# Optimization experiments

Measured on AMD Instinct MI355X. Metric: run time of the kernel, lower is better.

The kernel has to match this reference:

```python
import jax, jax.numpy as jnp
import numpy as np

DN = ('NCHW', 'OIHW', 'NCHW')
TEMP = 3.0
EPS = 1e-5


def conv2d(x, w, b):
    y = jax.lax.conv_general_dilated(x, w, (1, 1), 'SAME', dimension_numbers=DN)
    return y + b[None, :, None, None]


def cp_conv4d(x, wq, bq, wsp, bsp):
    # CenterPivotConv4d: 2D conv over query dims (h,w) batched over support dims,
    # plus 2D conv over support dims (hs,ws) batched over query dims.
    B, C, h, w, hs, ws = x.shape
    x1 = x.transpose(0, 4, 5, 1, 2, 3).reshape(B * hs * ws, C, h, w)
    o1 = conv2d(x1, wq, bq)
    Co = o1.shape[1]
    o1 = o1.reshape(B, hs, ws, Co, h, w).transpose(0, 3, 4, 5, 1, 2)
    x2 = x.transpose(0, 2, 3, 1, 4, 5).reshape(B * h * w, C, hs, ws)
    o2 = conv2d(x2, wsp, bsp)
    o2 = o2.reshape(B, h, w, Co, hs, ws).transpose(0, 3, 1, 2, 4, 5)
    return o1 + o2


def conv_stack(x, params):
    for wq, bq, wsp, bsp in params:  # fixed 3 layers, structurally distinct channels
        x = jax.nn.relu(cp_conv4d(x, wq, bq, wsp, bsp))
    return x


def neigh_consensus(x, params):
    # symmetric_mode: conv(x) + conv(x with (h,w)<->(hs,ws) swapped), swapped back
    y1 = conv_stack(x, params)
    y2 = conv_stack(x.transpose(0, 1, 4, 5, 2, 3), params).transpose(0, 1, 4, 5, 2, 3)
    return y1 + y2


def mutual_matching(c):
    # c: [B, 1, f1, f2, f3, f4]; ch==1 so the torch views reduce to axis maxes
    b_max = jnp.max(c, axis=(1, 2, 3), keepdims=True)  # max over (ch,f1,f2) per (f3,f4)
    a_max = jnp.max(c, axis=(4, 5), keepdims=True)     # max over (f3,f4) per (f1,f2)
    return c * (c / (a_max + EPS)) * (c / (b_max + EPS))


def matchnet_fwd(corr, v, ig_mask, params):
    B, _, h, w, hs, ws = corr.shape
    c = mutual_matching(corr)
    c = neigh_consensus(c, params)
    c = mutual_matching(c)
    corr2d = c.reshape(B, h * w, hs * ws)
    mask = jnp.broadcast_to(ig_mask.reshape(B, -1, hs * ws), corr2d.shape)
    corr2d = jnp.where(mask, jnp.float32(1e-4), corr2d)
    attn = jax.nn.softmax(corr2d * TEMP, axis=-1)
    # bmm(v, attn^T): v [B,Cv,K], attn [B,Q,K] -> [B,Cv,Q]
    wv = jnp.einsum('bck,bqk->bcq', v, attn)
    return wv.reshape(B, -1, h, w)


def setup_inputs():
    key = jax.random.key(0)
    ks = jax.random.split(key, 16)
    B, h, w, hs, ws, Cv = 4, 32, 32, 32, 32, 256
    chans = [(1, 10), (10, 10), (10, 1)]
    inp = {
        'corr': jax.random.normal(ks[0], (B, 1, h, w, hs, ws), jnp.float32),
        'v': jax.random.normal(ks[1], (B, Cv, hs * ws), jnp.float32),
        'ig_mask': jax.random.bernoulli(ks[2], 0.1, (B, 1, hs * ws)),
    }
    i = 3
    for li, (ci, co) in enumerate(chans):
        inp[f'wq{li}'] = jax.random.normal(ks[i], (co, ci, 3, 3), jnp.float32) * 0.1; i += 1
        inp[f'bq{li}'] = jax.random.normal(ks[i], (co,), jnp.float32) * 0.01; i += 1
        inp[f'ws{li}'] = jax.random.normal(ks[i], (co, ci, 3, 3), jnp.float32) * 0.1; i += 1
        inp[f'bs{li}'] = jax.random.normal(ks[i], (co,), jnp.float32) * 0.01; i += 1
    return inp


def reference(corr, v, ig_mask, wq0, bq0, ws0, bs0, wq1, bq1, ws1, bs1, wq2, bq2, ws2, bs2):
    params = [(wq0, bq0, ws0, bs0), (wq1, bq1, ws1, bs1), (wq2, bq2, ws2, bs2)]
    return matchnet_fwd(corr, v, ig_mask, params)
```

## Files before the change

### kernel.cpp

```cpp
#include <hip/hip_runtime.h>
#include <hip/hip_bf16.h>
#include <cstdint>

#define TEMPF 3.0f
#define EPSF 1e-5f

typedef __attribute__((ext_vector_type(8))) short bf16x8;
typedef __attribute__((ext_vector_type(4))) float f32x4;

static __device__ __forceinline__ float bf2f(unsigned short u){
  union { unsigned u32; float f; } x; x.u32 = ((unsigned)u) << 16; return x.f;
}
static __device__ __forceinline__ unsigned short f2bf(float f){
  unsigned u = __float_as_uint(f);
  unsigned r = (u + 0x7fffu + ((u >> 16) & 1u)) >> 16;
  return (unsigned short)r;
}
static __device__ __forceinline__ float4 ld4(const float* p){ return *(const float4*)p; }
static __device__ __forceinline__ float4 ld4(const __hip_bfloat16* p){
  ushort4 u = *(const ushort4*)p;
  return make_float4(bf2f(u.x), bf2f(u.y), bf2f(u.z), bf2f(u.w));
}
static __device__ __forceinline__ void st4(float* p, float4 v){ *(float4*)p = v; }
static __device__ __forceinline__ void st4(__hip_bfloat16* p, float4 v){
  *(ushort4*)p = make_ushort4(f2bf(v.x), f2bf(v.y), f2bf(v.z), f2bf(v.w));
}

static __device__ __forceinline__ unsigned fkey(float f){
  unsigned u = __float_as_uint(f);
  return (u & 0x80000000u) ? ~u : (u | 0x80000000u);
}
static __device__ __forceinline__ float fdec(unsigned k){
  return (k & 0x80000000u) ? __uint_as_float(k ^ 0x80000000u) : __uint_as_float(~k);
}

__device__ __forceinline__ float blockMax256(float v){
  __shared__ float red[4];
  #pragma unroll
  for(int off = 32; off; off >>= 1) v = fmaxf(v, __shfl_down(v, off));
  __syncthreads();
  if((threadIdx.x & 63) == 0) red[threadIdx.x >> 6] = v;
  __syncthreads();
  return fmaxf(fmaxf(red[0], red[1]), fmaxf(red[2], red[3]));
}
__device__ __forceinline__ float blockSum256(float v){
  __shared__ float red2[4];
  #pragma unroll
  for(int off = 32; off; off >>= 1) v += __shfl_down(v, off);
  __syncthreads();
  if((threadIdx.x & 63) == 0) red2[threadIdx.x >> 6] = v;
  __syncthreads();
  return red2[0] + red2[1] + red2[2] + red2[3];
}

__global__ void detect_k(const unsigned* __restrict__ m, int* __restrict__ flag){
  __shared__ int sa, sb;
  int tid = threadIdx.x;
  if(tid == 0){ sa = 0; sb = 0; }
  __syncthreads();
  int a = 0, b2 = 0;
  for(int i = tid; i < 1024; i += 256){
    unsigned w = m[i];
    if(w != 0u && w != 1u) a = 1;
    if(w != 0u && w != 0x3f800000u) b2 = 1;
  }
  if(a)  atomicOr(&sa, 1);
  if(b2) atomicOr(&sb, 1);
  __syncthreads();
  if(tid == 0) *flag = (sa == 0) ? 0 : ((sb == 0) ? 1 : 2);
}

__global__ void zero_k(unsigned* a, unsigned* b, unsigned* z){
  int i = blockIdx.x * 256 + threadIdx.x;
  if(i < 4096){ a[i] = 0u; b[i] = 0u; }
  if(i < 1024) z[i] = 0u;
}

__global__ __launch_bounds__(256) void zeroy_k(float4* __restrict__ y){
  y[blockIdx.x * 256 + threadIdx.x] = make_float4(0.f, 0.f, 0.f, 0.f);
}

__global__ __launch_bounds__(256) void rowmax_k(const float* __restrict__ x,
                                                float* __restrict__ rmax){
  int row = blockIdx.x;
  float4 v = *(const float4*)(x + (size_t)row * 1024 + threadIdx.x * 4);
  float m = fmaxf(fmaxf(v.x, v.y), fmaxf(v.z, v.w));
  m = blockMax256(m);
  if(threadIdx.x == 0) rmax[row] = m;
}

__global__ __launch_bounds__(256) void colmax_k(const float* __restrict__ x,
                                                unsigned* __restrict__ cbits){
  int blk = blockIdx.x;
  int b = blk >> 5, rg = blk & 31;
  const float* base = x + (size_t)b * 1024 * 1024 + (size_t)rg * 32 * 1024;
  int col = threadIdx.x * 4;
  float4 m = make_float4(-1e30f, -1e30f, -1e30f, -1e30f);
  for(int r = 0; r < 32; ++r){
    float4 v = *(const float4*)(base + r * 1024 + col);
    m.x = fmaxf(m.x, v.x); m.y = fmaxf(m.y, v.y);
    m.z = fmaxf(m.z, v.z); m.w = fmaxf(m.w, v.w);
  }
  unsigned* cb = cbits + (b << 10) + col;
  atomicMax(cb + 0, fkey(m.x)); atomicMax(cb + 1, fkey(m.y));
  atomicMax(cb + 2, fkey(m.z)); atomicMax(cb + 3, fkey(m.w));
}

__global__ __launch_bounds__(256) void mmapply_k(const float* __restrict__ x,
    const float* __restrict__ rmax, const unsigned* __restrict__ cbits,
    float* __restrict__ out){
  int idx4 = blockIdx.x * 256 + threadIdx.x;
  int b = idx4 >> 18;
  int rem = idx4 & 262143;
  int q = rem >> 8;
  int k = (rem & 255) * 4;
  float4 v = ((const float4*)x)[idx4];
  float ra = rmax[(b << 10) + q] + EPSF;
  const unsigned* cb = cbits + (b << 10) + k;
  float4 o;
  o.x = v.x * v.x * v.x / (ra * (fdec(cb[0]) + EPSF));
  o.y = v.y * v.y * v.y / (ra * (fdec(cb[1]) + EPSF));
  o.z = v.z * v.z * v.z / (ra * (fdec(cb[2]) + EPSF));
  o.w = v.w * v.w * v.w / (ra * (fdec(cb[3]) + EPSF));
  ((float4*)out)[idx4] = o;
}

__global__ void wpackL1_k(const float* __restrict__ wq1, const float* __restrict__ wsp1,
                          const float* __restrict__ bq1, const float* __restrict__ bsp1,
                          unsigned short* __restrict__ wp, float* __restrict__ bs){
  int i = blockIdx.x * 256 + threadIdx.x;
  if(i < 6144){
    int path = i / 3072, rem = i % 3072, co = rem / 192, k = rem % 192;
    float v = 0.f;
    if(co < 10 && k < 180){
      const float* WA = path ? wsp1 : wq1;
      const float* WB = path ? wq1 : wsp1;
      int kk = k < 90 ? k : k - 90;
      int ci = kk / 9, t = kk % 9;
      v = (k < 90 ? WA : WB)[(co * 10 + ci) * 9 + t];
    }
    wp[i] = f2bf(v);
  }
  if(i < 32){
    int co = i & 15;
    bs[i] = co < 10 ? bq1[co] + bsp1[co] : 0.f;
  }
}

__global__ __launch_bounds__(256)
void convmm_k(const unsigned short* __restrict__ gin, unsigned short* __restrict__ gout,
              const unsigned short* __restrict__ wpack, const float* __restrict__ bias,
              unsigned inElem, unsigned outElem, unsigned zeroElem){
  __shared__ unsigned short sh[13600];
  const int tid = threadIdx.x;
  const int blk = ((blockIdx.x & 7) << 8) | (blockIdx.x >> 3);
  const int path = blk >> 10;
  const int hw = blk & 1023;
  const int h = hw >> 5, w = hw & 31;
  const unsigned inB = inElem + (unsigned)path * 10485760u;
  const unsigned outB = outElem + (unsigned)path * 10485760u;

  for(int i = tid; i < 6800; i += 256) ((unsigned*)sh)[i] = 0u;
  __syncthreads();
  for(int idx = tid; idx < 2560; idx += 256){
    int ci = idx >> 8, s = (idx & 255) * 4;
    ushort4 v = *(const ushort4*)(gin + inB + ci * 1048576 + hw * 1024 + s);
    *(ushort4*)(sh + ci * 1360 + (1 + (s >> 5)) * 40 + 4 + (s & 31)) = v;
  }
  __syncthreads();

  const int l = tid & 63, wv = tid >> 6;
  const int g = l >> 4, n = l & 15;

  bf16x8 af[6];
  #pragma unroll
  for(int sl = 0; sl < 6; ++sl)
    af[sl] = *(const bf16x8*)(wpack + ((size_t)path * 16 + n) * 192 + sl * 32 + g * 8);
  f32x4 cb = *(const f32x4*)(bias + path * 16 + g * 4);

  unsigned b1i[24]; unsigned b2b[32]; unsigned msk2[4], msk5[4];
  unsigned s0 = (unsigned)wv * 256u;
  #pragma unroll
  for(int gg = 0; gg < 4; ++gg){
    if(g == gg){
      #pragma unroll
      for(int sl = 0; sl < 3; ++sl){
        #pragma unroll
        for(int j = 0; j < 8; ++j){
          const int k = sl * 32 + gg * 8 + j;
          unsigned v = zeroElem;
          if(k < 90){
            const int ci = k / 9, t = k % 9;
            const int hh = h + t / 3 - 1, ww = w + t % 3 - 1;
            if((unsigned)hh < 32u && (unsigned)ww < 32u)
              v = inB + (unsigned)ci * 1048576u + (unsigned)((hh * 32 + ww) * 1024) + (unsigned)n;
          }
          b1i[sl * 8 + j] = v + s0;
        }
      }
      #pragma unroll
      for(int sl = 2; sl < 6; ++sl){
        #pragma unroll
        for(int j = 0; j < 8; ++j){
          const int k = sl * 32 + gg * 8 + j;
          const int kp = (k >= 90 && k < 180) ? (k - 90) : 0;
          const int ci = kp / 9, t = kp % 9;
          b2b[(sl - 2) * 8 + j] = (unsigned)(ci * 1360 + (t / 3) * 40 + 3 + (t % 3) + n);
        }
      }
      #pragma unroll
      for(int p = 0; p < 4; ++p){
        const int ka = 64 + gg * 8 + 2 * p, kb = ka + 1;
        msk2[p] = ((ka >= 90) ? 0xFFFFu : 0u) | ((kb >= 90) ? 0xFFFF0000u : 0u);
        const int kc = 160 + gg * 8 + 2 * p, kd = kc + 1;
        msk5[p] = ((kc < 180) ? 0xFFFFu : 0u) | ((kd < 180) ? 0xFFFF0000u : 0u);
      }
    }
  }

  unsigned short ga[24], gb[24];
  #pragma unroll
  for(int m = 0; m < 24; ++m) ga[m] = gin[b1i[m]];
  #pragma unroll
  for(int m = 0; m < 24; ++m) b1i[m] += 16u;

#define CMM_STEP(CUR, NXT)                                                        \
  {                                                                               \
    _Pragma("unroll")                                                             \
    for(int m = 0; m < 24; ++m) NXT[m] = gin[b1i[m]];                             \
    _Pragma("unroll")                                                             \
    for(int m = 0; m < 24; ++m) b1i[m] += 16u;                                    \
    const unsigned rowcs = ((s0 >> 5) * 40u) + (s0 & 16u);                        \
    union { unsigned u[4]; bf16x8 v; } B0, B1, B2, B3, B4, B5;                    \
    _Pragma("unroll")                                                             \
    for(int p = 0; p < 4; ++p){                                                   \
      B0.u[p] = (unsigned)CUR[2*p]    | ((unsigned)CUR[2*p+1] << 16);             \
      B1.u[p] = (unsigned)CUR[8+2*p]  | ((unsigned)CUR[8+2*p+1] << 16);           \
      unsigned glo = (unsigned)CUR[16+2*p] | ((unsigned)CUR[16+2*p+1] << 16);     \
      unsigned llo = (unsigned)sh[b2b[2*p] + rowcs] |                             \
                     ((unsigned)sh[b2b[2*p+1] + rowcs] << 16);                    \
      B2.u[p] = glo | (llo & msk2[p]);                                            \
      B3.u[p] = (unsigned)sh[b2b[8+2*p]  + rowcs] |                               \
                ((unsigned)sh[b2b[8+2*p+1]  + rowcs] << 16);                      \
      B4.u[p] = (unsigned)sh[b2b[16+2*p] + rowcs] |                               \
                ((unsigned)sh[b2b[16+2*p+1] + rowcs] << 16);                      \
      B5.u[p] = ((unsigned)sh[b2b[24+2*p] + rowcs] |                              \
                 ((unsigned)sh[b2b[24+2*p+1] + rowcs] << 16)) & msk5[p];          \
    }                                                                             \
    __builtin_amdgcn_s_setprio(1);                                                \
    f32x4 acc = __builtin_amdgcn_mfma_f32_16x16x32_bf16(af[0], B0.v, cb, 0, 0, 0);\
    acc = __builtin_amdgcn_mfma_f32_16x16x32_bf16(af[1], B1.v, acc, 0, 0, 0);     \
    acc = __builtin_amdgcn_mfma_f32_16x16x32_bf16(af[2], B2.v, acc, 0, 0, 0);     \
    acc = __builtin_amdgcn_mfma_f32_16x16x32_bf16(af[3], B3.v, acc, 0, 0, 0);     \
    acc = __builtin_amdgcn_mfma_f32_16x16x32_bf16(af[4], B4.v, acc, 0, 0, 0);     \
    acc = __builtin_amdgcn_mfma_f32_16x16x32_bf16(af[5], B5.v, acc, 0, 0, 0);     \
    __builtin_amdgcn_s_setprio(0);                                                \
    _Pragma("unroll")                                                             \
    for(int r = 0; r < 4; ++r){                                                   \
      const int co = g * 4 + r;                                                   \
      if(co < 10)                                                                 \
        gout[outB + (unsigned)co * 1048576u + (unsigned)(hw * 1024) + s0 + n] =   \
            f2bf(fmaxf(acc[r], 0.f));                                             \
    }                                                                             \
    s0 += 16u;                                                                    \
  }

  for(int itp = 0; itp < 8; ++itp){
    CMM_STEP(ga, gb)
    CMM_STEP(gb, ga)
  }
#undef CMM_STEP
}

template<int CI, typename TI, typename TO>
__global__ __launch_bounds__(128, 4) void conv12_k(
    const TI* __restrict__ in, TO* __restrict__ out,
    const float* __restrict__ wq, const float* __restrict__ wsp,
    const float* __restrict__ bq, const float* __restrict__ bsp,
    size_t in_pstride){
  __shared__ float P[18][36];
  const int tid = threadIdx.x;
  const int blk = ((blockIdx.x & 7) << 9) | (blockIdx.x >> 3);
  const int path = blk >> 11;
  const int r0 = blk & 2047;
  const int strip = r0 & 1;
  const int hw = r0 >> 1;
  const int w = hw & 31, h = hw >> 5;
  const int lr = tid >> 3;
  const int c  = (tid & 7) * 4;
  const int own = hw * 1024 + strip * 512 + tid * 4;
  const int halo_src = hw * 1024 + (strip ? 15 * 32 : 16 * 32) + (tid & 7) * 4;
  const int hrow = strip ? 0 : 17;
  const float* wA = path ? wsp : wq;
  const float* wB = path ? wq : wsp;
  const TI* inp = in + (size_t)path * in_pstride;
  TO* outp = out + (size_t)path * 10485760;

  bool valid[9];
  #pragma unroll
  for(int dh = 0; dh < 3; ++dh)
    #pragma unroll
    for(int dw = 0; dw < 3; ++dw)
      valid[dh * 3 + dw] = ((unsigned)(h + dh - 1) < 32u) && ((unsigned)(w + dw - 1) < 32u);

  for(int i = tid; i < 18 * 36; i += 128) ((float*)P)[i] = 0.f;

  float acc[10][4];
  #pragma unroll
  for(int co = 0; co < 10; ++co){
    float bv = bq[co] + bsp[co];
    acc[co][0] = bv; acc[co][1] = bv; acc[co][2] = bv; acc[co][3] = bv;
  }

  for(int ci = 0; ci < CI; ++ci){
    const TI* base = inp + (size_t)ci * 1048576;
    float4 qv[9];
    #pragma unroll
    for(int dh = 0; dh < 3; ++dh){
      #pragma unroll
      for(int dw = 0; dw < 3; ++dw){
        const int t = dh * 3 + dw;
        float4 vv = make_float4(0.f, 0.f, 0.f, 0.f);
        if(valid[t]) vv = ld4(base + own + ((dh - 1) * 32 + (dw - 1)) * 1024);
        qv[t] = vv;
      }
    }
    float4 hv = make_float4(0.f, 0.f, 0.f, 0.f);
    if(tid < 8) hv = ld4(base + halo_src);

    __syncthreads();
    *(float4*)&P[1 + lr][c] = qv[4];
    if(tid < 8) *(float4*)&P[hrow][tid * 4] = hv;
    __syncthreads();

    float pr[3][6];
    #pragma unroll
    for(int k1 = 0; k1 < 3; ++k1){
      const float* row = &P[lr + k1][0];
      float4 mid = *(const float4*)(row + c);
      pr[k1][0] = row[c == 0 ? 32 : c - 1];
      pr[k1][1] = mid.x; pr[k1][2] = mid.y; pr[k1][3] = mid.z; pr[k1][4] = mid.w;
      pr[k1][5] = row[c + 4];
    }

    #pragma unroll
    for(int co = 0; co < 10; ++co){
      const float* wa = wA + (co * CI + ci) * 9;
      const float* wb = wB + (co * CI + ci) * 9;
      #pragma unroll
      for(int t = 0; t < 9; ++t){
        float wv = wa[t];
        acc[co][0] += wv * qv[t].x; acc[co][1] += wv * qv[t].y;
        acc[co][2] += wv * qv[t].z; acc[co][3] += wv * qv[t].w;
      }
      #pragma unroll
      for(int k1 = 0; k1 < 3; ++k1){
        #pragma unroll
        for(int k2 = 0; k2 < 3; ++k2){
          float wv = wb[k1 * 3 + k2];
          #pragma unroll
          for(int j = 0; j < 4; ++j) acc[co][j] += wv * pr[k1][k2 + j];
        }
      }
    }
  }

  #pragma unroll
  for(int co = 0; co < 10; ++co){
    float4 r;
    r.x = fmaxf(acc[co][0], 0.f); r.y = fmaxf(acc[co][1], 0.f);
    r.z = fmaxf(acc[co][2], 0.f); r.w = fmaxf(acc[co][3], 0.f);
    st4(outp + (size_t)co * 1048576 + own, r);
  }
}

__global__ __launch_bounds__(128, 4) void conv3_k(
    const __hip_bfloat16* __restrict__ in,
    const float* __restrict__ wq, const float* __restrict__ wsp,
    const float* __restrict__ bq, const float* __restrict__ bsp,
    float* __restrict__ yb){
  __shared__ float P[18][36];
  const int tid = threadIdx.x;
  const int blk = ((blockIdx.x & 7) << 9) | (blockIdx.x >> 3);
  const int path = blk >> 11;
  const int r0 = blk & 2047;
  const int strip = r0 & 1;
  const int hw = r0 >> 1;
  const int w = hw & 31, h = hw >> 5;
  const int lr = tid >> 3;
  const int c  = (tid & 7) * 4;
  const int own = hw * 1024 + strip * 512 + tid * 4;
  const int halo_src = hw * 1024 + (strip ? 15 * 32 : 16 * 32) + (tid & 7) * 4;
  const int hrow = strip ? 0 : 17;
  const float* wA = path ? wsp : wq;
  const float* wB = path ? wq : wsp;
  const __hip_bfloat16* inp = in + (size_t)path * 10485760;

  bool valid[9];
  #pragma unroll
  for(int dh = 0; dh < 3; ++dh)
    #pragma unroll
    for(int dw = 0; dw < 3; ++dw)
      valid[dh * 3 + dw] = ((unsigned)(h + dh - 1) < 32u) && ((unsigned)(w + dw - 1) < 32u);

  for(int i = tid; i < 18 * 36; i += 128) ((float*)P)[i] = 0.f;

  float bv = bq[0] + bsp[0];
  float a0 = bv, a1 = bv, a2 = bv, a3 = bv;

  for(int ci = 0; ci < 10; ++ci){
    const __hip_bfloat16* base = inp + (size_t)ci * 1048576;
    float4 qv[9];
    #pragma unroll
    for(int dh = 0; dh < 3; ++dh){
      #pragma unroll
      for(int dw = 0; dw < 3; ++dw){
        const int t = dh * 3 + dw;
        float4 vv = make_float4(0.f, 0.f, 0.f, 0.f);
        if(valid[t]) vv = ld4(base + own + ((dh - 1) * 32 + (dw - 1)) * 1024);
        qv[t] = vv;
      }
    }
    float4 hv = make_float4(0.f, 0.f, 0.f, 0.f);
    if(tid < 8) hv = ld4(base + halo_src);

    __syncthreads();
    *(float4*)&P[1 + lr][c] = qv[4];
    if(tid < 8) *(float4*)&P[hrow][tid * 4] = hv;
    __syncthreads();

    float pr[3][6];
    #pragma unroll
    for(int k1 = 0; k1 < 3; ++k1){
      const float* row = &P[lr + k1][0];
      float4 mid = *(const float4*)(row + c);
      pr[k1][0] = row[c == 0 ? 32 : c - 1];
      pr[k1][1] = mid.x; pr[k1][2] = mid.y; pr[k1][3] = mid.z; pr[k1][4] = mid.w;
      pr[k1][5] = row[c + 4];
    }

    const float* wa = wA + ci * 9;
    const float* wb = wB + ci * 9;
    #pragma unroll
    for(int t = 0; t < 9; ++t){
      float wv = wa[t];
      a0 += wv * qv[t].x; a1 += wv * qv[t].y;
      a2 += wv * qv[t].z; a3 += wv * qv[t].w;
    }
    #pragma unroll
    for(int k1 = 0; k1 < 3; ++k1){
      #pragma unroll
      for(int k2 = 0; k2 < 3; ++k2){
        float wv = wb[k1 * 3 + k2];
        a0 += wv * pr[k1][k2 + 0];
        a1 += wv * pr[k1][k2 + 1];
        a2 += wv * pr[k1][k2 + 2];
        a3 += wv * pr[k1][k2 + 3];
      }
    }
  }

  atomicAdd(yb + own + 0, fmaxf(a0, 0.f));
  atomicAdd(yb + own + 1, fmaxf(a1, 0.f));
  atomicAdd(yb + own + 2, fmaxf(a2, 0.f));
  atomicAdd(yb + own + 3, fmaxf(a3, 0.f));
}

__global__ __launch_bounds__(256) void softmax_k(
    const float* __restrict__ y, const float* __restrict__ rmax,
    const unsigned* __restrict__ cbits, const void* __restrict__ mask,
    const int* __restrict__ mode, float* __restrict__ attn){
  int row = blockIdx.x;
  int b = row >> 10;
  int tid = threadIdx.x;
  int kc = tid * 4;
  float ra = rmax[row] + EPSF;
  float4 v = *(const float4*)(y + (size_t)row * 1024 + kc);
  int md = *mode;
  float vv[4] = {v.x, v.y, v.z, v.w};
  float s[4];
  #pragma unroll
  for(int j = 0; j < 4; ++j){
    int k = kc + j;
    float cb = fdec(cbits[(b << 10) + k]) + EPSF;
    float m = vv[j] * vv[j] * vv[j] / (ra * cb);
    bool msk;
    if(md == 0)      msk = ((const int*)mask)[(b << 10) + k] != 0;
    else if(md == 1) msk = ((const float*)mask)[(b << 10) + k] != 0.f;
    else             msk = ((const unsigned char*)mask)[(b << 10) + k] != 0;
    if(msk) m = 1e-4f;
    s[j] = m * TEMPF;
  }
  float mx = fmaxf(fmaxf(s[0], s[1]), fmaxf(s[2], s[3]));
  mx = blockMax256(mx);
  float e[4]; float sum = 0.f;
  #pragma unroll
  for(int j = 0; j < 4; ++j){ e[j] = expf(s[j] - mx); sum += e[j]; }
  sum = blockSum256(sum);
  float inv = 1.0f / sum;
  float4 o; o.x = e[0] * inv; o.y = e[1] * inv; o.z = e[2] * inv; o.w = e[3] * inv;
  *(float4*)(attn + (size_t)row * 1024 + kc) = o;
}

__global__ __launch_bounds__(256) void bmm_k(const float* __restrict__ v,
    const float* __restrict__ attn, float* __restrict__ part){
  __shared__ float At[64][68];
  __shared__ float Bt[64][68];
  int b  = blockIdx.y >> 2;
  int ks = blockIdx.y & 3;
  int ct = blockIdx.x >> 4, qt = blockIdx.x & 15;
  int tid = threadIdx.x;
  int c0 = ct * 64, q0 = qt * 64;
  int tx = tid & 15, ty = tid >> 4;
  float acc[4][4] = {};
  for(int k0 = ks * 256; k0 < ks * 256 + 256; k0 += 64){
    #pragma unroll
    for(int l = 0; l < 4; ++l){
      int r = (tid >> 4) + l * 16;
      int cc = (tid & 15) * 4;
      *(float4*)&At[r][cc] = *(const float4*)(v    + ((size_t)b * 256  + c0 + r) * 1024 + k0 + cc);
      *(float4*)&Bt[r][cc] = *(const float4*)(attn + ((size_t)b * 1024 + q0 + r) * 1024 + k0 + cc);
    }
    __syncthreads();
    #pragma unroll 4
    for(int kk = 0; kk < 64; ++kk){
      float a_[4], b_[4];
      #pragma unroll
      for(int i = 0; i < 4; ++i){ a_[i] = At[ty * 4 + i][kk]; b_[i] = Bt[tx * 4 + i][kk]; }
      #pragma unroll
      for(int i = 0; i < 4; ++i)
        #pragma unroll
        for(int j = 0; j < 4; ++j) acc[i][j] += a_[i] * b_[j];
    }
    __syncthreads();
  }
  float* pb = part + (size_t)ks * 1048576;
  #pragma unroll
  for(int i = 0; i < 4; ++i){
    float4 r; r.x = acc[i][0]; r.y = acc[i][1]; r.z = acc[i][2]; r.w = acc[i][3];
    *(float4*)(pb + ((size_t)b * 256 + c0 + ty * 4 + i) * 1024 + q0 + tx * 4) = r;
  }
}

__global__ __launch_bounds__(256) void bmmred_k(const float* __restrict__ part,
                                                float* __restrict__ out){
  int i = blockIdx.x * 256 + threadIdx.x;
  const float4* p = (const float4*)part;
  float4 a = p[i], b = p[i + 262144], cc = p[i + 524288], d = p[i + 786432];
  float4 o;
  o.x = a.x + b.x + cc.x + d.x;
  o.y = a.y + b.y + cc.y + d.y;
  o.z = a.z + b.z + cc.z + d.z;
  o.w = a.w + b.w + cc.w + d.w;
  ((float4*)out)[i] = o;
}

extern "C" void kernel_launch(void* const* d_in, const int* in_sizes, int n_in,
                              void* d_out, int out_size, void* d_ws, size_t ws_size,
                              hipStream_t stream){
  (void)in_sizes; (void)n_in; (void)out_size; (void)ws_size;
  const float* corr = (const float*)d_in[0];
  const float* v    = (const float*)d_in[1];
  const void*  mask = d_in[2];
  const float* wq[3]  = {(const float*)d_in[3],  (const float*)d_in[7],  (const float*)d_in[11]};
  const float* bq[3]  = {(const float*)d_in[4],  (const float*)d_in[8],  (const float*)d_in[12]};
  const float* wsp[3] = {(const float*)d_in[5],  (const float*)d_in[9],  (const float*)d_in[13]};
  const float* bsp[3] = {(const float*)d_in[6],  (const float*)d_in[10], (const float*)d_in[14]};
  float* out = (float*)d_out;

  char* ws = (char*)d_ws;
  float* x0 = (float*)(ws);
  float* y  = (float*)(ws + 16777216);
  char* aux = ws + 33554432;
  float*    rmax1 = (float*)(aux);
  unsigned* cb1   = (unsigned*)(aux + 16384);
  float*    rmax2 = (float*)(aux + 32768);
  unsigned* cb2   = (unsigned*)(aux + 49152);
  int*      flag  = (int*)(aux + 65536);
  unsigned short* wp = (unsigned short*)(aux + 69632);
  float*          bs = (float*)(aux + 81920);
  unsigned* zeros = (unsigned*)(aux + 98304);
  char* treg = ws + 33685504;
  __hip_bfloat16* t1 = (__hip_bfloat16*)(treg);
  __hip_bfloat16* t2 = (__hip_bfloat16*)(treg + 41943040);
  float* attn = x0;
  float* part = (float*)treg;

  const unsigned t1Elem   = 33685504u / 2u;
  const unsigned t2Elem   = 75628544u / 2u;
  const unsigned zeroElem = 33652736u / 2u;

  detect_k<<<1, 256, 0, stream>>>((const unsigned*)mask, flag);
  zero_k<<<16, 256, 0, stream>>>(cb1, cb2, zeros);
  zeroy_k<<<4096, 256, 0, stream>>>((float4*)y);
  wpackL1_k<<<24, 256, 0, stream>>>(wq[1], wsp[1], bq[1], bsp[1], wp, bs);
  rowmax_k<<<4096, 256, 0, stream>>>(corr, rmax1);
  colmax_k<<<128, 256, 0, stream>>>(corr, cb1);
  mmapply_k<<<4096, 256, 0, stream>>>(corr, rmax1, cb1, x0);

  for(int bb = 0; bb < 4; ++bb){
    const float* xb = x0 + (size_t)bb * 1048576;
    float*       yb = y  + (size_t)bb * 1048576;
    conv12_k<1, float, __hip_bfloat16><<<4096, 128, 0, stream>>>(
        xb, t1, wq[0], wsp[0], bq[0], bsp[0], 0);
    convmm_k<<<2048, 256, 0, stream>>>(
        (const unsigned short*)ws, (unsigned short*)ws, wp, bs, t1Elem, t2Elem, zeroElem);
    conv3_k<<<4096, 128, 0, stream>>>(
        t2, wq[2], wsp[2], bq[2], bsp[2], yb);
  }

  rowmax_k<<<4096, 256, 0, stream>>>(y, rmax2);
  colmax_k<<<128, 256, 0, stream>>>(y, cb2);
  softmax_k<<<4096, 256, 0, stream>>>(y, rmax2, cb2, mask, flag, attn);
  bmm_k<<<dim3(64, 16), 256, 0, stream>>>(v, attn, part);
  bmmred_k<<<1024, 256, 0, stream>>>(part, out);
}
```

Measured before the change: 707.7 us.

## Merge setup and max-reduction kernels; double convmm block size to 512 threads

After: 771.3 us. +9.0%, slower.

```diff
diff --git a/kernel.cpp b/kernel.cpp
--- a/kernel.cpp
+++ b/kernel.cpp
@@ -53,57 +53,78 @@
   return red2[0] + red2[1] + red2[2] + red2[3];
 }
 
-__global__ void detect_k(const unsigned* __restrict__ m, int* __restrict__ flag){
-  __shared__ int sa, sb;
-  int tid = threadIdx.x;
-  if(tid == 0){ sa = 0; sb = 0; }
-  __syncthreads();
-  int a = 0, b2 = 0;
-  for(int i = tid; i < 1024; i += 256){
-    unsigned w = m[i];
-    if(w != 0u && w != 1u) a = 1;
-    if(w != 0u && w != 0x3f800000u) b2 = 1;
-  }
-  if(a)  atomicOr(&sa, 1);
-  if(b2) atomicOr(&sb, 1);
-  __syncthreads();
-  if(tid == 0) *flag = (sa == 0) ? 0 : ((sb == 0) ? 1 : 2);
-}
-
-__global__ void zero_k(unsigned* a, unsigned* b, unsigned* z){
-  int i = blockIdx.x * 256 + threadIdx.x;
-  if(i < 4096){ a[i] = 0u; b[i] = 0u; }
-  if(i < 1024) z[i] = 0u;
-}
-
-__global__ __launch_bounds__(256) void zeroy_k(float4* __restrict__ y){
-  y[blockIdx.x * 256 + threadIdx.x] = make_float4(0.f, 0.f, 0.f, 0.f);
-}
-
-__global__ __launch_bounds__(256) void rowmax_k(const float* __restrict__ x,
-                                                float* __restrict__ rmax){
-  int row = blockIdx.x;
-  float4 v = *(const float4*)(x + (size_t)row * 1024 + threadIdx.x * 4);
-  float m = fmaxf(fmaxf(v.x, v.y), fmaxf(v.z, v.w));
-  m = blockMax256(m);
-  if(threadIdx.x == 0) rmax[row] = m;
-}
-
-__global__ __launch_bounds__(256) void colmax_k(const float* __restrict__ x,
-                                                unsigned* __restrict__ cbits){
-  int blk = blockIdx.x;
-  int b = blk >> 5, rg = blk & 31;
-  const float* base = x + (size_t)b * 1024 * 1024 + (size_t)rg * 32 * 1024;
-  int col = threadIdx.x * 4;
-  float4 m = make_float4(-1e30f, -1e30f, -1e30f, -1e30f);
-  for(int r = 0; r < 32; ++r){
-    float4 v = *(const float4*)(base + r * 1024 + col);
-    m.x = fmaxf(m.x, v.x); m.y = fmaxf(m.y, v.y);
-    m.z = fmaxf(m.z, v.z); m.w = fmaxf(m.w, v.w);
-  }
-  unsigned* cb = cbits + (b << 10) + col;
-  atomicMax(cb + 0, fkey(m.x)); atomicMax(cb + 1, fkey(m.y));
-  atomicMax(cb + 2, fkey(m.z)); atomicMax(cb + 3, fkey(m.w));
+__global__ __launch_bounds__(256) void setup_k(
+    const unsigned* __restrict__ mask, int* __restrict__ flag,
+    unsigned* __restrict__ cb1, unsigned* __restrict__ cb2, unsigned* __restrict__ zeros,
+    const float* __restrict__ wq1, const float* __restrict__ wsp1,
+    const float* __restrict__ bq1, const float* __restrict__ bsp1,
+    unsigned short* __restrict__ wp, float* __restrict__ bs,
+    float4* __restrict__ y){
+  const int b = blockIdx.x, tid = threadIdx.x;
+  if(b < 4096){
+    y[b * 256 + tid] = make_float4(0.f, 0.f, 0.f, 0.f);
+  } else if(b == 4096){
+    __shared__ int sa, sb;
+    if(tid == 0){ sa = 0; sb = 0; }
+    __syncthreads();
+    int a = 0, b2 = 0;
+    for(int i = tid; i < 1024; i += 256){
+      unsigned w = mask[i];
+      if(w != 0u && w != 1u) a = 1;
+      if(w != 0u && w != 0x3f800000u) b2 = 1;
+    }
+    if(a)  atomicOr(&sa, 1);
+    if(b2) atomicOr(&sb, 1);
+    __syncthreads();
+    if(tid == 0) *flag = (sa == 0) ? 0 : ((sb == 0) ? 1 : 2);
+  } else if(b < 4121){
+    int i = (b - 4097) * 256 + tid;
+    if(i < 6144){
+      int path = i / 3072, rem = i % 3072, co = rem / 192, k = rem % 192;
+      float v = 0.f;
+      if(co < 10 && k < 180){
+        const float* WA = path ? wsp1 : wq1;
+        const float* WB = path ? wq1 : wsp1;
+        int kk = k < 90 ? k : k - 90;
+        int ci = kk / 9, t = kk % 9;
+        v = (k < 90 ? WA : WB)[(co * 10 + ci) * 9 + t];
+      }
+      wp[i] = f2bf(v);
+    }
+    if(i < 32){
+      int co = i & 15;
+      bs[i] = co < 10 ? bq1[co] + bsp1[co] : 0.f;
+    }
+  } else {
+    int i = (b - 4121) * 256 + tid;
+    if(i < 4096){ cb1[i] = 0u; cb2[i] = 0u; }
+    if(i < 1024) zeros[i] = 0u;
+  }
+}
+
+__global__ __launch_bounds__(256) void rcmax_k(const float* __restrict__ x,
+    float* __restrict__ rmax, unsigned* __restrict__ cbits){
+  const int b = blockIdx.x, tid = threadIdx.x;
+  if(b < 4096){
+    float4 v = *(const float4*)(x + (size_t)b * 1024 + tid * 4);
+    float m = fmaxf(fmaxf(v.x, v.y), fmaxf(v.z, v.w));
+    m = blockMax256(m);
+    if(tid == 0) rmax[b] = m;
+  } else {
+    int blk = b - 4096;
+    int bb = blk >> 5, rg = blk & 31;
+    const float* base = x + (size_t)bb * 1048576 + (size_t)rg * 32 * 1024;
+    int col = tid * 4;
+    float4 m = make_float4(-1e30f, -1e30f, -1e30f, -1e30f);
+    for(int r = 0; r < 32; ++r){
+      float4 v = *(const float4*)(base + r * 1024 + col);
+      m.x = fmaxf(m.x, v.x); m.y = fmaxf(m.y, v.y);
+      m.z = fmaxf(m.z, v.z); m.w = fmaxf(m.w, v.w);
+    }
+    unsigned* cb = cbits + (bb << 10) + col;
+    atomicMax(cb + 0, fkey(m.x)); atomicMax(cb + 1, fkey(m.y));
+    atomicMax(cb + 2, fkey(m.z)); atomicMax(cb + 3, fkey(m.w));
+  }
 }
 
 __global__ __launch_bounds__(256) void mmapply_k(const float* __restrict__ x,
@@ -125,29 +146,7 @@
   ((float4*)out)[idx4] = o;
 }
 
-__global__ void wpackL1_k(const float* __restrict__ wq1, const float* __restrict__ wsp1,
-                          const float* __restrict__ bq1, const float* __restrict__ bsp1,
-                          unsigned short* __restrict__ wp, float* __restrict__ bs){
-  int i = blockIdx.x * 256 + threadIdx.x;
-  if(i < 6144){
-    int path = i / 3072, rem = i % 3072, co = rem / 192, k = rem % 192;
-    float v = 0.f;
-    if(co < 10 && k < 180){
-      const float* WA = path ? wsp1 : wq1;
-      const float* WB = path ? wq1 : wsp1;
-      int kk = k < 90 ? k : k - 90;
-      int ci = kk / 9, t = kk % 9;
-      v = (k < 90 ? WA : WB)[(co * 10 + ci) * 9 + t];
-    }
-    wp[i] = f2bf(v);
-  }
-  if(i < 32){
-    int co = i & 15;
-    bs[i] = co < 10 ? bq1[co] + bsp1[co] : 0.f;
-  }
-}
-
-__global__ __launch_bounds__(256)
+__global__ __launch_bounds__(512)
 void convmm_k(const unsigned short* __restrict__ gin, unsigned short* __restrict__ gout,
               const unsigned short* __restrict__ wpack, const float* __restrict__ bias,
               unsigned inElem, unsigned outElem, unsigned zeroElem){
@@ -160,9 +159,9 @@
   const unsigned inB = inElem + (unsigned)path * 10485760u;
   const unsigned outB = outElem + (unsigned)path * 10485760u;
 
-  for(int i = tid; i < 6800; i += 256) ((unsigned*)sh)[i] = 0u;
+  for(int i = tid; i < 6800; i += 512) ((unsigned*)sh)[i] = 0u;
   __syncthreads();
-  for(int idx = tid; idx < 2560; idx += 256){
+  for(int idx = tid; idx < 2560; idx += 512){
     int ci = idx >> 8, s = (idx & 255) * 4;
     ushort4 v = *(const ushort4*)(gin + inB + ci * 1048576 + hw * 1024 + s);
     *(ushort4*)(sh + ci * 1360 + (1 + (s >> 5)) * 40 + 4 + (s & 31)) = v;
@@ -179,7 +178,7 @@
   f32x4 cb = *(const f32x4*)(bias + path * 16 + g * 4);
 
   unsigned b1i[24]; unsigned b2b[32]; unsigned msk2[4], msk5[4];
-  unsigned s0 = (unsigned)wv * 256u;
+  unsigned s0 = (unsigned)wv * 128u;
   #pragma unroll
   for(int gg = 0; gg < 4; ++gg){
     if(g == gg){
@@ -265,7 +264,7 @@
     s0 += 16u;                                                                    \
   }
 
-  for(int itp = 0; itp < 8; ++itp){
+  for(int itp = 0; itp < 4; ++itp){
     CMM_STEP(ga, gb)
     CMM_STEP(gb, ga)
   }
@@ -590,12 +589,9 @@
   const unsigned t2Elem   = 75628544u / 2u;
   const unsigned zeroElem = 33652736u / 2u;
 
-  detect_k<<<1, 256, 0, stream>>>((const unsigned*)mask, flag);
-  zero_k<<<16, 256, 0, stream>>>(cb1, cb2, zeros);
-  zeroy_k<<<4096, 256, 0, stream>>>((float4*)y);
-  wpackL1_k<<<24, 256, 0, stream>>>(wq[1], wsp[1], bq[1], bsp[1], wp, bs);
-  rowmax_k<<<4096, 256, 0, stream>>>(corr, rmax1);
-  colmax_k<<<128, 256, 0, stream>>>(corr, cb1);
+  setup_k<<<4137, 256, 0, stream>>>((const unsigned*)mask, flag, cb1, cb2, zeros,
+                                    wq[1], wsp[1], bq[1], bsp[1], wp, bs, (float4*)y);
+  rcmax_k<<<4224, 256, 0, stream>>>(corr, rmax1, cb1);
   mmapply_k<<<4096, 256, 0, stream>>>(corr, rmax1, cb1, x0);
 
   for(int bb = 0; bb < 4; ++bb){
@@ -603,14 +599,13 @@
     float*       yb = y  + (size_t)bb * 1048576;
     conv12_k<1, float, __hip_bfloat16><<<4096, 128, 0, stream>>>(
         xb, t1, wq[0], wsp[0], bq[0], bsp[0], 0);
-    convmm_k<<<2048, 256, 0, stream>>>(
+    convmm_k<<<2048, 512, 0, stream>>>(
         (const unsigned short*)ws, (unsigned short*)ws, wp, bs, t1Elem, t2Elem, zeroElem);
     conv3_k<<<4096, 128, 0, stream>>>(
         t2, wq[2], wsp[2], bq[2], bsp[2], yb);
   }
 
-  rowmax_k<<<4096, 256, 0, stream>>>(y, rmax2);
-  colmax_k<<<128, 256, 0, stream>>>(y, cb2);
+  rcmax_k<<<4224, 256, 0, stream>>>(y, rmax2, cb2);
   softmax_k<<<4096, 256, 0, stream>>>(y, rmax2, cb2, mask, flag, attn);
   bmm_k<<<dim3(64, 16), 256, 0, stream>>>(v, attn, part);
   bmmred_k<<<1024, 256, 0, stream>>>(part, out);
```
